# Performance work log

Measured on AMD Instinct MI355X. Metric: run time of the kernel, lower is better.

## Reference

```python
import jax, jax.numpy as jnp
import numpy as np

B, M, T = 4, 80, 65536
R, D, S, L = 64, 64, 64, 20  # residual, dilation, skip channels; num_layers


def setup_inputs() -> dict:
    key = jax.random.key(0)
    ks = jax.random.split(key, 14)

    def w(k, shape, fan_in):
        return jax.random.normal(k, shape, jnp.float32) * (1.0 / np.sqrt(fan_in))

    return {
        "x": jax.random.normal(ks[0], (B, M, T), jnp.float32),
        # causal 1x1 conv: Conv1d(M, R, 1) -> weight [R, M]
        "w_causal": w(ks[1], (R, M), M),
        "b_causal": jnp.zeros((R,), jnp.float32),
        # per-layer stacked weights (kernel_size=1 so all convs are channel matmuls)
        "w_dil": w(ks[2], (L, D, R), R),
        "b_dil": jnp.zeros((L, D), jnp.float32),
        "w_res": w(ks[3], (L, R, D), D),
        "b_res": jnp.zeros((L, R), jnp.float32),
        "w_skip": w(ks[4], (L, S, D), D),
        "b_skip": jnp.zeros((L, S), jnp.float32),
        "w_post1": w(ks[5], (S, S), S),
        "b_post1": jnp.zeros((S,), jnp.float32),
        "w_post2": w(ks[6], (1, S), S),
        "b_post2": jnp.zeros((1,), jnp.float32),
    }


def reference(x, w_causal, b_causal, w_dil, b_dil, w_res, b_res,
              w_skip, b_skip, w_post1, b_post1, w_post2, b_post2):
    # initial 1x1 conv: [B,M,T] -> [B,R,T]
    h = jnp.einsum('rm,bmt->brt', w_causal, x) + b_causal[None, :, None]

    skip0 = jnp.zeros((x.shape[0], w_skip.shape[1], x.shape[2]), x.dtype)

    def layer(carry, params):
        h, skip_sum = carry
        wd, bd, wr, br, ws, bs = params
        f = jnp.tanh(jnp.einsum('dr,brt->bdt', wd, h) + bd[None, :, None])
        skip_sum = skip_sum + jnp.einsum('sd,bdt->bst', ws, f) + bs[None, :, None]
        h = h + jnp.einsum('rd,bdt->brt', wr, f) + br[None, :, None]
        return (h, skip_sum), None

    (h, skip_sum), _ = jax.lax.scan(
        layer, (h, skip0), (w_dil, b_dil, w_res, b_res, w_skip, b_skip))

    s = jnp.tanh(skip_sum)
    s = jnp.tanh(jnp.einsum('os,bst->bot', w_post1, s) + b_post1[None, :, None])
    out = jnp.einsum('os,bst->bot', w_post2, s) + b_post2[None, :, None]
    return out[:, 0, :]  # squeeze channel dim -> [B, T]
```

## Files before the change

kernel.cpp:

```cpp
#include <hip/hip_runtime.h>

#define NB 4
#define NM 80
#define NT 65536
#define NL 20

typedef __bf16 bf16x8 __attribute__((ext_vector_type(8), may_alias));
typedef float f32x4 __attribute__((ext_vector_type(4), may_alias));
typedef unsigned int u32x2 __attribute__((ext_vector_type(2), may_alias));
typedef unsigned int u32x4 __attribute__((ext_vector_type(4), may_alias));

#define WCHI 491520
#define WCLO 497664
#define W1HI 503808
#define W1LO 507904

__device__ __forceinline__ unsigned f2u(float x) { return __float_as_uint(x); }
__device__ __forceinline__ float u2f(unsigned u) { return __uint_as_float(u); }
__device__ __forceinline__ unsigned pack2(float a, float b) {
    return (f2u(a) >> 16) | (f2u(b) & 0xffff0000u);
}
__device__ __forceinline__ unsigned rne_hi(float a) {
    unsigned u = f2u(a);
    return (u + 0x7fffu + ((u >> 16) & 1u)) & 0xffff0000u;
}
__device__ __forceinline__ unsigned pack2_rne(float a, float b) {
    return (rne_hi(a) >> 16) | rne_hi(b);
}
__device__ __forceinline__ float fast_tanh(float v) {
    float e = __expf(2.0f * v);
    return 1.0f - 2.0f / (e + 1.0f);
}
__device__ __forceinline__ f32x4 mm3(bf16x8 ah, bf16x8 al, bf16x8 bh, bf16x8 bl, f32x4 c) {
    c = __builtin_amdgcn_mfma_f32_16x16x32_bf16(ah, bh, c, 0, 0, 0);
    c = __builtin_amdgcn_mfma_f32_16x16x32_bf16(ah, bl, c, 0, 0, 0);
    c = __builtin_amdgcn_mfma_f32_16x16x32_bf16(al, bh, c, 0, 0, 0);
    return c;
}
__device__ __forceinline__ f32x4 mm2(bf16x8 ah, bf16x8 al, bf16x8 b, f32x4 c) {
    c = __builtin_amdgcn_mfma_f32_16x16x32_bf16(ah, b, c, 0, 0, 0);
    c = __builtin_amdgcn_mfma_f32_16x16x32_bf16(al, b, c, 0, 0, 0);
    return c;
}
__device__ __forceinline__ void split_pack(f32x4 v, u32x2& hi, u32x2& lo) {
    float l0 = v[0] - u2f(f2u(v[0]) & 0xffff0000u);
    float l1 = v[1] - u2f(f2u(v[1]) & 0xffff0000u);
    float l2 = v[2] - u2f(f2u(v[2]) & 0xffff0000u);
    float l3 = v[3] - u2f(f2u(v[3]) & 0xffff0000u);
    hi[0] = pack2(v[0], v[1]);
    hi[1] = pack2(v[2], v[3]);
    lo[0] = pack2(l0, l1);
    lo[1] = pack2(l2, l3);
}
__device__ __forceinline__ unsigned shf(unsigned v, int sl) {
    return (unsigned)__shfl((int)v, sl, 64);
}
__device__ __forceinline__ u32x4 gatherB(u32x2 p0, u32x2 p1, int slA, int slB, bool hiSel) {
    unsigned a0 = shf(p0[0], slA), b0 = shf(p1[0], slA);
    unsigned a1 = shf(p0[1], slA), b1 = shf(p1[1], slA);
    unsigned a2 = shf(p0[0], slB), b2 = shf(p1[0], slB);
    unsigned a3 = shf(p0[1], slB), b3 = shf(p1[1], slB);
    u32x4 r;
    r[0] = hiSel ? b0 : a0;
    r[1] = hiSel ? b1 : a1;
    r[2] = hiSel ? b2 : a2;
    r[3] = hiSel ? b3 : a3;
    return r;
}
__device__ __forceinline__ bf16x8 asbf(const u32x4& v) { return *(const bf16x8*)&v; }

__device__ __forceinline__ void stage_phase(const unsigned short* __restrict__ wsu,
                                            unsigned short* lbase, int pg, int wave, int lane) {
#pragma unroll
    for (int jj = 0; jj < 4; ++jj) {
        const unsigned short* g = wsu + (size_t)pg * 8192 + (wave * 4 + jj) * 512 + lane * 8;
        unsigned short* lp = lbase + (wave * 4 + jj) * 512;
        __builtin_amdgcn_global_load_lds(
            (const __attribute__((address_space(1))) unsigned int*)g,
            (__attribute__((address_space(3))) unsigned int*)lp, 16, 0, 0);
    }
}

#define PHASE_SYNC() do { \
    asm volatile("s_waitcnt vmcnt(0)" ::: "memory"); \
    __builtin_amdgcn_s_barrier(); \
} while (0)

extern "C" __global__ void __launch_bounds__(256)
wavenet_prep(const float* __restrict__ wc, const float* __restrict__ wd,
             const float* __restrict__ wsk, const float* __restrict__ wr,
             const float* __restrict__ w1, unsigned short* __restrict__ o)
{
    int i = blockIdx.x * 256 + threadIdx.x;
    if (i < 491520) {
        int pg = i >> 13;
        int within = i & 8191;
        int c = within >> 9;
        int lam = (within >> 3) & 63;
        int j = i & 7;
        int plane = c >> 3, m = (c >> 1) & 3, ks = c & 1;
        int row = m * 16 + (lam & 15);
        int k = ks * 32 + (lam >> 4) * 8 + j;
        int l = pg / 3, p = pg - 3 * l;
        const float* W = (p == 0) ? wd : (p == 1) ? wsk : wr;
        float v = W[(l * 64 + row) * 64 + k];
        unsigned uh = f2u(v) & 0xffff0000u;
        unsigned val = plane ? (f2u(v - u2f(uh)) >> 16) : (uh >> 16);
        o[i] = (unsigned short)val;
    } else if (i < 497664) {
        int idx = i - 491520;
        int r = idx / 96, mm = idx - r * 96;
        float v = (mm < NM) ? wc[r * NM + mm] : 0.0f;
        unsigned uh = f2u(v) & 0xffff0000u;
        o[WCHI + idx] = (unsigned short)(uh >> 16);
        o[WCLO + idx] = (unsigned short)(f2u(v - u2f(uh)) >> 16);
    } else if (i < 501760) {
        int idx = i - 497664;
        float v = w1[idx];
        unsigned uh = f2u(v) & 0xffff0000u;
        o[W1HI + idx] = (unsigned short)(uh >> 16);
        o[W1LO + idx] = (unsigned short)(f2u(v - u2f(uh)) >> 16);
    }
}

extern "C" __global__ void __launch_bounds__(256)
wavenet_mfma(const float* __restrict__ x, const float* __restrict__ bc,
             const float* __restrict__ bd, const float* __restrict__ br,
             const float* __restrict__ bs, const float* __restrict__ b1,
             const float* __restrict__ w2, const float* __restrict__ b2,
             const unsigned short* __restrict__ wsu, float* __restrict__ out)
{
    __shared__ __align__(16) unsigned short wbuf[2][8192];

    const int tid = threadIdx.x;
    const int wave = tid >> 6;
    const int lane = tid & 63;
    const int q = lane >> 4;
    const int c16 = lane & 15;
    const int wcol0 = wave * 32;

    const int slA = ((lane & 16) << 1) + c16;
    const int slB = slA + 16;
    const bool hiSel = lane >= 32;

    const int gcol0 = blockIdx.x * 128;
    const int bidx = gcol0 >> 16;
    const float* xbase = x + (size_t)bidx * NM * NT + (gcol0 & (NT - 1));

    stage_phase(wsu, &wbuf[0][0], 0, wave, lane);

    f32x4 h[4][2];
    f32x4 skipacc[4][2];
#pragma unroll
    for (int m = 0; m < 4; ++m)
#pragma unroll
        for (int nt = 0; nt < 2; ++nt)
            skipacc[m][nt] = (f32x4){0.f, 0.f, 0.f, 0.f};

#pragma unroll
    for (int nt = 0; nt < 2; ++nt) {
        const int colL = wcol0 + nt * 16 + c16;
        const float* xcp = xbase + colL;

        bf16x8 Bh[3], Bl[3];
#pragma unroll
        for (int ks = 0; ks < 3; ++ks) {
            u32x4 ph, pl;
#pragma unroll
            for (int w = 0; w < 4; ++w) {
                const int m0 = ks * 32 + q * 8 + 2 * w;
                float a, bv;
                if (ks < 2) {
                    a  = xcp[(size_t)m0 * NT];
                    bv = xcp[(size_t)(m0 + 1) * NT];
                } else {
                    const int ma = (m0 < NM) ? m0 : 0;
                    const int mb = (m0 + 1 < NM) ? (m0 + 1) : 0;
                    a  = (m0 < NM) ? xcp[(size_t)ma * NT] : 0.0f;
                    bv = (m0 + 1 < NM) ? xcp[(size_t)mb * NT] : 0.0f;
                }
                const float la = a - u2f(f2u(a) & 0xffff0000u);
                const float lb = bv - u2f(f2u(bv) & 0xffff0000u);
                ph[w] = pack2(a, bv);
                pl[w] = pack2(la, lb);
            }
            Bh[ks] = asbf(ph);
            Bl[ks] = asbf(pl);
        }

#pragma unroll
        for (int m = 0; m < 4; ++m) {
            f32x4 acc = *(const f32x4*)(bc + m * 16 + q * 4);
#pragma unroll
            for (int ks = 0; ks < 3; ++ks) {
                bf16x8 Ah = *(const bf16x8*)(wsu + WCHI + (m * 16 + c16) * 96 + ks * 32 + q * 8);
                bf16x8 Al = *(const bf16x8*)(wsu + WCLO + (m * 16 + c16) * 96 + ks * 32 + q * 8);
                acc = mm3(Ah, Al, Bh[ks], Bl[ks], acc);
            }
            h[m][nt] = acc;
        }
    }

    int buf = 0;
#pragma unroll 1
    for (int l = 0; l < NL; ++l) {
        const float* bdl = bd + l * 64;
        const float* brl = br + l * 64;

        PHASE_SYNC();
        stage_phase(wsu, &wbuf[buf ^ 1][0], 3 * l + 1, wave, lane);
        {
            const unsigned short* wb = &wbuf[buf][0];

            u32x4 BhH[2][2], BlH[2][2];
#pragma unroll
            for (int nt = 0; nt < 2; ++nt) {
                u32x2 Ph[4], Pl[4];
#pragma unroll
                for (int m = 0; m < 4; ++m) split_pack(h[m][nt], Ph[m], Pl[m]);
#pragma unroll
                for (int ks = 0; ks < 2; ++ks) {
                    BhH[nt][ks] = gatherB(Ph[ks * 2], Ph[ks * 2 + 1], slA, slB, hiSel);
                    BlH[nt][ks] = gatherB(Pl[ks * 2], Pl[ks * 2 + 1], slA, slB, hiSel);
                }
            }

            u32x2 Pf[2][4];
#pragma unroll
            for (int m = 0; m < 4; ++m) {
                bf16x8 Ah[2], Al[2];
#pragma unroll
                for (int ks = 0; ks < 2; ++ks) {
                    Ah[ks] = *(const bf16x8*)(wb + (m * 2 + ks) * 512 + lane * 8);
                    Al[ks] = *(const bf16x8*)(wb + (8 * 8 + (m * 2 + ks) * 8 - 8 * 8 + 8 * 512 / 512 * 0 + (8 + m * 2 + ks) * 512 - (m * 2 + ks) * 512 - 512 * 8) * 0 + (8 + m * 2 + ks) * 512 + lane * 8);
                }
                f32x4 bd4 = *(const f32x4*)(bdl + m * 16 + q * 4);
#pragma unroll
                for (int nt = 0; nt < 2; ++nt) {
                    f32x4 acc = bd4;
#pragma unroll
                    for (int ks = 0; ks < 2; ++ks)
                        acc = mm3(Ah[ks], Al[ks], asbf(BhH[nt][ks]), asbf(BlH[nt][ks]), acc);
                    Pf[nt][m][0] = pack2_rne(fast_tanh(acc[0]), fast_tanh(acc[1]));
                    Pf[nt][m][1] = pack2_rne(fast_tanh(acc[2]), fast_tanh(acc[3]));
                }
            }
            buf ^= 1;

            u32x4 BF[2][2];
#pragma unroll
            for (int nt = 0; nt < 2; ++nt)
#pragma unroll
                for (int ks = 0; ks < 2; ++ks)
                    BF[nt][ks] = gatherB(Pf[nt][ks * 2], Pf[nt][ks * 2 + 1], slA, slB, hiSel);

            PHASE_SYNC();
            stage_phase(wsu, &wbuf[buf ^ 1][0], 3 * l + 2, wave, lane);
            wb = &wbuf[buf][0];
#pragma unroll
            for (int m = 0; m < 4; ++m) {
                bf16x8 Ah[2], Al[2];
#pragma unroll
                for (int ks = 0; ks < 2; ++ks) {
                    Ah[ks] = *(const bf16x8*)(wb + (m * 2 + ks) * 512 + lane * 8);
                    Al[ks] = *(const bf16x8*)(wb + (8 + m * 2 + ks) * 512 + lane * 8);
                }
#pragma unroll
                for (int nt = 0; nt < 2; ++nt)
#pragma unroll
                    for (int ks = 0; ks < 2; ++ks)
                        skipacc[m][nt] = mm2(Ah[ks], Al[ks], asbf(BF[nt][ks]), skipacc[m][nt]);
            }
            buf ^= 1;

            PHASE_SYNC();
            if (l < NL - 1)
                stage_phase(wsu, &wbuf[buf ^ 1][0], 3 * l + 3, wave, lane);
            wb = &wbuf[buf][0];
#pragma unroll
            for (int m = 0; m < 4; ++m) {
                bf16x8 Ah[2], Al[2];
#pragma unroll
                for (int ks = 0; ks < 2; ++ks) {
                    Ah[ks] = *(const bf16x8*)(wb + (m * 2 + ks) * 512 + lane * 8);
                    Al[ks] = *(const bf16x8*)(wb + (8 + m * 2 + ks) * 512 + lane * 8);
                }
                f32x4 br4 = *(const f32x4*)(brl + m * 16 + q * 4);
#pragma unroll
                for (int nt = 0; nt < 2; ++nt) {
                    f32x4 c = h[m][nt];
#pragma unroll
                    for (int i = 0; i < 4; ++i) c[i] += br4[i];
#pragma unroll
                    for (int ks = 0; ks < 2; ++ks)
                        c = mm2(Ah[ks], Al[ks], asbf(BF[nt][ks]), c);
                    h[m][nt] = c;
                }
            }
            buf ^= 1;
        }
    }

    u32x2 Ps[2][4];
#pragma unroll
    for (int m = 0; m < 4; ++m) {
        f32x4 bsum = (f32x4){0.f, 0.f, 0.f, 0.f};
#pragma unroll
        for (int l = 0; l < NL; ++l) {
            f32x4 bv = *(const f32x4*)(bs + l * 64 + m * 16 + q * 4);
#pragma unroll
            for (int i = 0; i < 4; ++i) bsum[i] += bv[i];
        }
#pragma unroll
        for (int nt = 0; nt < 2; ++nt) {
            Ps[nt][m][0] = pack2_rne(fast_tanh(skipacc[m][nt][0] + bsum[0]),
                                     fast_tanh(skipacc[m][nt][1] + bsum[1]));
            Ps[nt][m][1] = pack2_rne(fast_tanh(skipacc[m][nt][2] + bsum[2]),
                                     fast_tanh(skipacc[m][nt][3] + bsum[3]));
        }
    }
    u32x4 BS[2][2];
#pragma unroll
    for (int nt = 0; nt < 2; ++nt)
#pragma unroll
        for (int ks = 0; ks < 2; ++ks)
            BS[nt][ks] = gatherB(Ps[nt][ks * 2], Ps[nt][ks * 2 + 1], slA, slB, hiSel);

    f32x4 s2a[4][2];
#pragma unroll
    for (int m = 0; m < 4; ++m) {
        bf16x8 Ah[2], Al[2];
#pragma unroll
        for (int ks = 0; ks < 2; ++ks) {
            Ah[ks] = *(const bf16x8*)(wsu + W1HI + (m * 16 + c16) * 64 + ks * 32 + q * 8);
            Al[ks] = *(const bf16x8*)(wsu + W1LO + (m * 16 + c16) * 64 + ks * 32 + q * 8);
        }
        f32x4 b14 = *(const f32x4*)(b1 + m * 16 + q * 4);
#pragma unroll
        for (int nt = 0; nt < 2; ++nt) {
            f32x4 acc = b14;
#pragma unroll
            for (int ks = 0; ks < 2; ++ks)
                acc = mm2(Ah[ks], Al[ks], asbf(BS[nt][ks]), acc);
#pragma unroll
            for (int i = 0; i < 4; ++i) s2a[m][nt][i] = fast_tanh(acc[i]);
        }
    }

    f32x4 w24[4];
#pragma unroll
    for (int m = 0; m < 4; ++m) w24[m] = *(const f32x4*)(w2 + m * 16 + q * 4);
    const float b2v = b2[0];
#pragma unroll
    for (int nt = 0; nt < 2; ++nt) {
        float p = 0.0f;
#pragma unroll
        for (int m = 0; m < 4; ++m)
#pragma unroll
            for (int i = 0; i < 4; ++i)
                p = fmaf(w24[m][i], s2a[m][nt][i], p);
        p += __shfl_xor(p, 16);
        p += __shfl_xor(p, 32);
        if (q == 0)
            out[gcol0 + wcol0 + nt * 16 + c16] = b2v + p;
    }
}

extern "C" void kernel_launch(void* const* d_in, const int* in_sizes, int n_in,
                              void* d_out, int out_size, void* d_ws, size_t ws_size,
                              hipStream_t stream) {
    const float* x  = (const float*)d_in[0];
    const float* wc = (const float*)d_in[1];
    const float* bc = (const float*)d_in[2];
    const float* wd = (const float*)d_in[3];
    const float* bd = (const float*)d_in[4];
    const float* wr = (const float*)d_in[5];
    const float* br = (const float*)d_in[6];
    const float* ws = (const float*)d_in[7];
    const float* bs = (const float*)d_in[8];
    const float* w1 = (const float*)d_in[9];
    const float* b1 = (const float*)d_in[10];
    const float* w2 = (const float*)d_in[11];
    const float* b2 = (const float*)d_in[12];
    float* out = (float*)d_out;
    unsigned short* wsu = (unsigned short*)d_ws;

    hipLaunchKernelGGL(wavenet_prep, dim3(1960), dim3(256), 0, stream,
                       wc, wd, ws, wr, w1, wsu);
    hipLaunchKernelGGL(wavenet_mfma, dim3((NB * NT) / 128), dim3(256), 0, stream,
                       x, bc, bd, br, bs, b1, w2, b2, wsu, out);
}
```

Measured before the change: 645.0 us.

## Halve per-wave column tile, use hardware bf16 pack, raise waves per EU

Each wave now handles 16 time columns instead of 32, so the block covers 64 columns and the grid doubles. This cuts register-resident h/skip accumulators in half so more waves can be resident (with an amdgpu_waves_per_eu hint), trading away reuse of the weight fragments loaded from shared memory across two column tiles. The hi/lo split now uses v_cvt_pk_bf16_f32 (round-to-nearest hi) instead of truncation masks. Weight staging into LDS per block is now amortized over half as many columns, increasing LDS traffic and barrier count per output.

```diff
diff --git a/kernel.cpp b/kernel.cpp
--- a/kernel.cpp
+++ b/kernel.cpp
@@ -26,6 +26,11 @@
 }
 __device__ __forceinline__ unsigned pack2_rne(float a, float b) {
     return (rne_hi(a) >> 16) | rne_hi(b);
+}
+__device__ __forceinline__ unsigned cvtpk(float a, float b) {
+    unsigned r;
+    asm("v_cvt_pk_bf16_f32 %0, %1, %2" : "=v"(r) : "v"(a), "v"(b));
+    return r;
 }
 __device__ __forceinline__ float fast_tanh(float v) {
     float e = __expf(2.0f * v);
@@ -43,14 +48,14 @@
     return c;
 }
 __device__ __forceinline__ void split_pack(f32x4 v, u32x2& hi, u32x2& lo) {
-    float l0 = v[0] - u2f(f2u(v[0]) & 0xffff0000u);
-    float l1 = v[1] - u2f(f2u(v[1]) & 0xffff0000u);
-    float l2 = v[2] - u2f(f2u(v[2]) & 0xffff0000u);
-    float l3 = v[3] - u2f(f2u(v[3]) & 0xffff0000u);
-    hi[0] = pack2(v[0], v[1]);
-    hi[1] = pack2(v[2], v[3]);
-    lo[0] = pack2(l0, l1);
-    lo[1] = pack2(l2, l3);
+    hi[0] = cvtpk(v[0], v[1]);
+    hi[1] = cvtpk(v[2], v[3]);
+    float r0 = v[0] - u2f(hi[0] << 16);
+    float r1 = v[1] - u2f(hi[0] & 0xffff0000u);
+    float r2 = v[2] - u2f(hi[1] << 16);
+    float r3 = v[3] - u2f(hi[1] & 0xffff0000u);
+    lo[0] = cvtpk(r0, r1);
+    lo[1] = cvtpk(r2, r3);
 }
 __device__ __forceinline__ unsigned shf(unsigned v, int sl) {
     return (unsigned)__shfl((int)v, sl, 64);
@@ -124,6 +129,7 @@
 }
 
 extern "C" __global__ void __launch_bounds__(256)
+__attribute__((amdgpu_waves_per_eu(3, 4)))
 wavenet_mfma(const float* __restrict__ x, const float* __restrict__ bc,
              const float* __restrict__ bd, const float* __restrict__ br,
              const float* __restrict__ bs, const float* __restrict__ b1,
@@ -137,29 +143,25 @@
     const int lane = tid & 63;
     const int q = lane >> 4;
     const int c16 = lane & 15;
-    const int wcol0 = wave * 32;
+    const int wcol0 = wave * 16;
 
     const int slA = ((lane & 16) << 1) + c16;
     const int slB = slA + 16;
     const bool hiSel = lane >= 32;
 
-    const int gcol0 = blockIdx.x * 128;
+    const int gcol0 = blockIdx.x * 64;
     const int bidx = gcol0 >> 16;
     const float* xbase = x + (size_t)bidx * NM * NT + (gcol0 & (NT - 1));
 
     stage_phase(wsu, &wbuf[0][0], 0, wave, lane);
 
-    f32x4 h[4][2];
-    f32x4 skipacc[4][2];
-#pragma unroll
-    for (int m = 0; m < 4; ++m)
-#pragma unroll
-        for (int nt = 0; nt < 2; ++nt)
-            skipacc[m][nt] = (f32x4){0.f, 0.f, 0.f, 0.f};
-
-#pragma unroll
-    for (int nt = 0; nt < 2; ++nt) {
-        const int colL = wcol0 + nt * 16 + c16;
+    f32x4 h[4];
+    f32x4 skipacc[4];
+#pragma unroll
+    for (int m = 0; m < 4; ++m) skipacc[m] = (f32x4){0.f, 0.f, 0.f, 0.f};
+
+    {
+        const int colL = wcol0 + c16;
         const float* xcp = xbase + colL;
 
         bf16x8 Bh[3], Bl[3];
@@ -197,7 +199,7 @@
                 bf16x8 Al = *(const bf16x8*)(wsu + WCLO + (m * 16 + c16) * 96 + ks * 32 + q * 8);
                 acc = mm3(Ah, Al, Bh[ks], Bl[ks], acc);
             }
-            h[m][nt] = acc;
+            h[m] = acc;
         }
     }
 
@@ -212,47 +214,40 @@
         {
             const unsigned short* wb = &wbuf[buf][0];
 
-            u32x4 BhH[2][2], BlH[2][2];
-#pragma unroll
-            for (int nt = 0; nt < 2; ++nt) {
+            u32x4 BhH[2], BlH[2];
+            {
                 u32x2 Ph[4], Pl[4];
 #pragma unroll
-                for (int m = 0; m < 4; ++m) split_pack(h[m][nt], Ph[m], Pl[m]);
+                for (int m = 0; m < 4; ++m) split_pack(h[m], Ph[m], Pl[m]);
 #pragma unroll
                 for (int ks = 0; ks < 2; ++ks) {
-                    BhH[nt][ks] = gatherB(Ph[ks * 2], Ph[ks * 2 + 1], slA, slB, hiSel);
-                    BlH[nt][ks] = gatherB(Pl[ks * 2], Pl[ks * 2 + 1], slA, slB, hiSel);
-                }
-            }
-
-            u32x2 Pf[2][4];
+                    BhH[ks] = gatherB(Ph[ks * 2], Ph[ks * 2 + 1], slA, slB, hiSel);
+                    BlH[ks] = gatherB(Pl[ks * 2], Pl[ks * 2 + 1], slA, slB, hiSel);
+                }
+            }
+
+            u32x2 Pf[4];
 #pragma unroll
             for (int m = 0; m < 4; ++m) {
                 bf16x8 Ah[2], Al[2];
 #pragma unroll
                 for (int ks = 0; ks < 2; ++ks) {
                     Ah[ks] = *(const bf16x8*)(wb + (m * 2 + ks) * 512 + lane * 8);
-                    Al[ks] = *(const bf16x8*)(wb + (8 * 8 + (m * 2 + ks) * 8 - 8 * 8 + 8 * 512 / 512 * 0 + (8 + m * 2 + ks) * 512 - (m * 2 + ks) * 512 - 512 * 8) * 0 + (8 + m * 2 + ks) * 512 + lane * 8);
-                }
-                f32x4 bd4 = *(const f32x4*)(bdl + m * 16 + q * 4);
-#pragma unroll
-                for (int nt = 0; nt < 2; ++nt) {
-                    f32x4 acc = bd4;
-#pragma unroll
-                    for (int ks = 0; ks < 2; ++ks)
-                        acc = mm3(Ah[ks], Al[ks], asbf(BhH[nt][ks]), asbf(BlH[nt][ks]), acc);
-                    Pf[nt][m][0] = pack2_rne(fast_tanh(acc[0]), fast_tanh(acc[1]));
-                    Pf[nt][m][1] = pack2_rne(fast_tanh(acc[2]), fast_tanh(acc[3]));
-                }
+                    Al[ks] = *(const bf16x8*)(wb + (8 + m * 2 + ks) * 512 + lane * 8);
+                }
+                f32x4 acc = *(const f32x4*)(bdl + m * 16 + q * 4);
+#pragma unroll
+                for (int ks = 0; ks < 2; ++ks)
+                    acc = mm3(Ah[ks], Al[ks], asbf(BhH[ks]), asbf(BlH[ks]), acc);
+                Pf[m][0] = pack2_rne(fast_tanh(acc[0]), fast_tanh(acc[1]));
+                Pf[m][1] = pack2_rne(fast_tanh(acc[2]), fast_tanh(acc[3]));
             }
             buf ^= 1;
 
-            u32x4 BF[2][2];
-#pragma unroll
-            for (int nt = 0; nt < 2; ++nt)
-#pragma unroll
-                for (int ks = 0; ks < 2; ++ks)
-                    BF[nt][ks] = gatherB(Pf[nt][ks * 2], Pf[nt][ks * 2 + 1], slA, slB, hiSel);
+            u32x4 BF[2];
+#pragma unroll
+            for (int ks = 0; ks < 2; ++ks)
+                BF[ks] = gatherB(Pf[ks * 2], Pf[ks * 2 + 1], slA, slB, hiSel);
 
             PHASE_SYNC();
             stage_phase(wsu, &wbuf[buf ^ 1][0], 3 * l + 2, wave, lane);
@@ -266,10 +261,8 @@
                     Al[ks] = *(const bf16x8*)(wb + (8 + m * 2 + ks) * 512 + lane * 8);
                 }
 #pragma unroll
-                for (int nt = 0; nt < 2; ++nt)
-#pragma unroll
-                    for (int ks = 0; ks < 2; ++ks)
-                        skipacc[m][nt] = mm2(Ah[ks], Al[ks], asbf(BF[nt][ks]), skipacc[m][nt]);
+                for (int ks = 0; ks < 2; ++ks)
+                    skipacc[m] = mm2(Ah[ks], Al[ks], asbf(BF[ks]), skipacc[m]);
             }
             buf ^= 1;
 
@@ -286,22 +279,19 @@
                     Al[ks] = *(const bf16x8*)(wb + (8 + m * 2 + ks) * 512 + lane * 8);
                 }
                 f32x4 br4 = *(const f32x4*)(brl + m * 16 + q * 4);
-#pragma unroll
-                for (int nt = 0; nt < 2; ++nt) {
-                    f32x4 c = h[m][nt];
-#pragma unroll
-                    for (int i = 0; i < 4; ++i) c[i] += br4[i];
-#pragma unroll
-                    for (int ks = 0; ks < 2; ++ks)
-                        c = mm2(Ah[ks], Al[ks], asbf(BF[nt][ks]), c);
-                    h[m][nt] = c;
-                }
+                f32x4 c = h[m];
+#pragma unroll
+                for (int i = 0; i < 4; ++i) c[i] += br4[i];
+#pragma unroll
+                for (int ks = 0; ks < 2; ++ks)
+                    c = mm2(Ah[ks], Al[ks], asbf(BF[ks]), c);
+                h[m] = c;
             }
             buf ^= 1;
         }
     }
 
-    u32x2 Ps[2][4];
+    u32x2 Ps[4];
 #pragma unroll
     for (int m = 0; m < 4; ++m) {
         f32x4 bsum = (f32x4){0.f, 0.f, 0.f, 0.f};
@@ -311,22 +301,17 @@
 #pragma unroll
             for (int i = 0; i < 4; ++i) bsum[i] += bv[i];
         }
-#pragma unroll
-        for (int nt = 0; nt < 2; ++nt) {
-            Ps[nt][m][0] = pack2_rne(fast_tanh(skipacc[m][nt][0] + bsum[0]),
-                                     fast_tanh(skipacc[m][nt][1] + bsum[1]));
-            Ps[nt][m][1] = pack2_rne(fast_tanh(skipacc[m][nt][2] + bsum[2]),
-                                     fast_tanh(skipacc[m][nt][3] + bsum[3]));
-        }
-    }
-    u32x4 BS[2][2];
-#pragma unroll
-    for (int nt = 0; nt < 2; ++nt)
-#pragma unroll
-        for (int ks = 0; ks < 2; ++ks)
-            BS[nt][ks] = gatherB(Ps[nt][ks * 2], Ps[nt][ks * 2 + 1], slA, slB, hiSel);
-
-    f32x4 s2a[4][2];
+        Ps[m][0] = pack2_rne(fast_tanh(skipacc[m][0] + bsum[0]),
+                             fast_tanh(skipacc[m][1] + bsum[1]));
+        Ps[m][1] = pack2_rne(fast_tanh(skipacc[m][2] + bsum[2]),
+                             fast_tanh(skipacc[m][3] + bsum[3]));
+    }
+    u32x4 BS[2];
+#pragma unroll
+    for (int ks = 0; ks < 2; ++ks)
+        BS[ks] = gatherB(Ps[ks * 2], Ps[ks * 2 + 1], slA, slB, hiSel);
+
+    f32x4 s2a[4];
 #pragma unroll
     for (int m = 0; m < 4; ++m) {
         bf16x8 Ah[2], Al[2];
@@ -335,35 +320,28 @@
             Ah[ks] = *(const bf16x8*)(wsu + W1HI + (m * 16 + c16) * 64 + ks * 32 + q * 8);
             Al[ks] = *(const bf16x8*)(wsu + W1LO + (m * 16 + c16) * 64 + ks * 32 + q * 8);
         }
-        f32x4 b14 = *(const f32x4*)(b1 + m * 16 + q * 4);
-#pragma unroll
-        for (int nt = 0; nt < 2; ++nt) {
-            f32x4 acc = b14;
-#pragma unroll
-            for (int ks = 0; ks < 2; ++ks)
-                acc = mm2(Ah[ks], Al[ks], asbf(BS[nt][ks]), acc);
-#pragma unroll
-            for (int i = 0; i < 4; ++i) s2a[m][nt][i] = fast_tanh(acc[i]);
-        }
+        f32x4 acc = *(const f32x4*)(b1 + m * 16 + q * 4);
+#pragma unroll
+        for (int ks = 0; ks < 2; ++ks)
+            acc = mm2(Ah[ks], Al[ks], asbf(BS[ks]), acc);
+#pragma unroll
+        for (int i = 0; i < 4; ++i) s2a[m][i] = fast_tanh(acc[i]);
     }
 
     f32x4 w24[4];
 #pragma unroll
     for (int m = 0; m < 4; ++m) w24[m] = *(const f32x4*)(w2 + m * 16 + q * 4);
     const float b2v = b2[0];
-#pragma unroll
-    for (int nt = 0; nt < 2; ++nt) {
-        float p = 0.0f;
-#pragma unroll
-        for (int m = 0; m < 4; ++m)
-#pragma unroll
-            for (int i = 0; i < 4; ++i)
-                p = fmaf(w24[m][i], s2a[m][nt][i], p);
-        p += __shfl_xor(p, 16);
-        p += __shfl_xor(p, 32);
-        if (q == 0)
-            out[gcol0 + wcol0 + nt * 16 + c16] = b2v + p;
-    }
+    float p = 0.0f;
+#pragma unroll
+    for (int m = 0; m < 4; ++m)
+#pragma unroll
+        for (int i = 0; i < 4; ++i)
+            p = fmaf(w24[m][i], s2a[m][i], p);
+    p += __shfl_xor(p, 16);
+    p += __shfl_xor(p, 32);
+    if (q == 0)
+        out[gcol0 + wcol0 + c16] = b2v + p;
 }
 
 extern "C" void kernel_launch(void* const* d_in, const int* in_sizes, int n_in,
@@ -387,6 +365,6 @@
 
     hipLaunchKernelGGL(wavenet_prep, dim3(1960), dim3(256), 0, stream,
                        wc, wd, ws, wr, w1, wsu);
-    hipLaunchKernelGGL(wavenet_mfma, dim3((NB * NT) / 128), dim3(256), 0, stream,
+    hipLaunchKernelGGL(wavenet_mfma, dim3((NB * NT) / 64), dim3(256), 0, stream,
                        x, bc, bd, br, bs, b1, w2, b2, wsu, out);
 }
```

After: 677.1 us. 1.05x slower.

## Use hardware bf16 packing, drop skip low-plane MFMAs, raise occupancy bound

Applied to the files above, without the earlier changes.

The hi/lo split now uses the hardware v_cvt_pk_bf16_f32 conversion, and the weight prep rounds to nearest even instead of truncating. With the high part rounded, dropping the low plane of the skip weights costs less accuracy. The skip-projection phase therefore stages only the high plane and does one MFMA per tile instead of two. Launch bounds now request 4 blocks per CU. This cuts MFMA count, LDS traffic and ALU work for splitting, at the cost of lower precision in the skip path and more register pressure from the occupancy hint.

```diff
diff --git a/kernel.cpp b/kernel.cpp
--- a/kernel.cpp
+++ b/kernel.cpp
@@ -26,6 +26,11 @@
 }
 __device__ __forceinline__ unsigned pack2_rne(float a, float b) {
     return (rne_hi(a) >> 16) | rne_hi(b);
+}
+__device__ __forceinline__ unsigned cvtpk(float a, float b) {
+    unsigned r;
+    asm("v_cvt_pk_bf16_f32 %0, %1, %2" : "=v"(r) : "v"(a), "v"(b));
+    return r;
 }
 __device__ __forceinline__ float fast_tanh(float v) {
     float e = __expf(2.0f * v);
@@ -43,14 +48,14 @@
     return c;
 }
 __device__ __forceinline__ void split_pack(f32x4 v, u32x2& hi, u32x2& lo) {
-    float l0 = v[0] - u2f(f2u(v[0]) & 0xffff0000u);
-    float l1 = v[1] - u2f(f2u(v[1]) & 0xffff0000u);
-    float l2 = v[2] - u2f(f2u(v[2]) & 0xffff0000u);
-    float l3 = v[3] - u2f(f2u(v[3]) & 0xffff0000u);
-    hi[0] = pack2(v[0], v[1]);
-    hi[1] = pack2(v[2], v[3]);
-    lo[0] = pack2(l0, l1);
-    lo[1] = pack2(l2, l3);
+    hi[0] = cvtpk(v[0], v[1]);
+    hi[1] = cvtpk(v[2], v[3]);
+    float r0 = v[0] - u2f(hi[0] << 16);
+    float r1 = v[1] - u2f(hi[0] & 0xffff0000u);
+    float r2 = v[2] - u2f(hi[1] << 16);
+    float r3 = v[3] - u2f(hi[1] & 0xffff0000u);
+    lo[0] = cvtpk(r0, r1);
+    lo[1] = cvtpk(r2, r3);
 }
 __device__ __forceinline__ unsigned shf(unsigned v, int sl) {
     return (unsigned)__shfl((int)v, sl, 64);
@@ -69,12 +74,13 @@
 }
 __device__ __forceinline__ bf16x8 asbf(const u32x4& v) { return *(const bf16x8*)&v; }
 
+template <int NCH>
 __device__ __forceinline__ void stage_phase(const unsigned short* __restrict__ wsu,
                                             unsigned short* lbase, int pg, int wave, int lane) {
 #pragma unroll
-    for (int jj = 0; jj < 4; ++jj) {
-        const unsigned short* g = wsu + (size_t)pg * 8192 + (wave * 4 + jj) * 512 + lane * 8;
-        unsigned short* lp = lbase + (wave * 4 + jj) * 512;
+    for (int jj = 0; jj < NCH; ++jj) {
+        const unsigned short* g = wsu + (size_t)pg * 8192 + (wave * NCH + jj) * 512 + lane * 8;
+        unsigned short* lp = lbase + (wave * NCH + jj) * 512;
         __builtin_amdgcn_global_load_lds(
             (const __attribute__((address_space(1))) unsigned int*)g,
             (__attribute__((address_space(3))) unsigned int*)lp, 16, 0, 0);
@@ -104,26 +110,26 @@
         int l = pg / 3, p = pg - 3 * l;
         const float* W = (p == 0) ? wd : (p == 1) ? wsk : wr;
         float v = W[(l * 64 + row) * 64 + k];
-        unsigned uh = f2u(v) & 0xffff0000u;
+        unsigned uh = rne_hi(v);
         unsigned val = plane ? (f2u(v - u2f(uh)) >> 16) : (uh >> 16);
         o[i] = (unsigned short)val;
     } else if (i < 497664) {
         int idx = i - 491520;
         int r = idx / 96, mm = idx - r * 96;
         float v = (mm < NM) ? wc[r * NM + mm] : 0.0f;
-        unsigned uh = f2u(v) & 0xffff0000u;
+        unsigned uh = rne_hi(v);
         o[WCHI + idx] = (unsigned short)(uh >> 16);
         o[WCLO + idx] = (unsigned short)(f2u(v - u2f(uh)) >> 16);
     } else if (i < 501760) {
         int idx = i - 497664;
         float v = w1[idx];
-        unsigned uh = f2u(v) & 0xffff0000u;
+        unsigned uh = rne_hi(v);
         o[W1HI + idx] = (unsigned short)(uh >> 16);
         o[W1LO + idx] = (unsigned short)(f2u(v - u2f(uh)) >> 16);
     }
 }
 
-extern "C" __global__ void __launch_bounds__(256)
+extern "C" __global__ void __launch_bounds__(256, 4)
 wavenet_mfma(const float* __restrict__ x, const float* __restrict__ bc,
              const float* __restrict__ bd, const float* __restrict__ br,
              const float* __restrict__ bs, const float* __restrict__ b1,
@@ -147,7 +153,7 @@
     const int bidx = gcol0 >> 16;
     const float* xbase = x + (size_t)bidx * NM * NT + (gcol0 & (NT - 1));
 
-    stage_phase(wsu, &wbuf[0][0], 0, wave, lane);
+    stage_phase<4>(wsu, &wbuf[0][0], 0, wave, lane);
 
     f32x4 h[4][2];
     f32x4 skipacc[4][2];
@@ -208,7 +214,7 @@
         const float* brl = br + l * 64;
 
         PHASE_SYNC();
-        stage_phase(wsu, &wbuf[buf ^ 1][0], 3 * l + 1, wave, lane);
+        stage_phase<2>(wsu, &wbuf[buf ^ 1][0], 3 * l + 1, wave, lane);
         {
             const unsigned short* wb = &wbuf[buf][0];
 
@@ -232,7 +238,7 @@
 #pragma unroll
                 for (int ks = 0; ks < 2; ++ks) {
                     Ah[ks] = *(const bf16x8*)(wb + (m * 2 + ks) * 512 + lane * 8);
-                    Al[ks] = *(const bf16x8*)(wb + (8 * 8 + (m * 2 + ks) * 8 - 8 * 8 + 8 * 512 / 512 * 0 + (8 + m * 2 + ks) * 512 - (m * 2 + ks) * 512 - 512 * 8) * 0 + (8 + m * 2 + ks) * 512 + lane * 8);
+                    Al[ks] = *(const bf16x8*)(wb + (8 + m * 2 + ks) * 512 + lane * 8);
                 }
                 f32x4 bd4 = *(const f32x4*)(bdl + m * 16 + q * 4);
 #pragma unroll
@@ -255,27 +261,26 @@
                     BF[nt][ks] = gatherB(Pf[nt][ks * 2], Pf[nt][ks * 2 + 1], slA, slB, hiSel);
 
             PHASE_SYNC();
-            stage_phase(wsu, &wbuf[buf ^ 1][0], 3 * l + 2, wave, lane);
+            stage_phase<4>(wsu, &wbuf[buf ^ 1][0], 3 * l + 2, wave, lane);
             wb = &wbuf[buf][0];
 #pragma unroll
             for (int m = 0; m < 4; ++m) {
-                bf16x8 Ah[2], Al[2];
-#pragma unroll
-                for (int ks = 0; ks < 2; ++ks) {
+                bf16x8 Ah[2];
+#pragma unroll
+                for (int ks = 0; ks < 2; ++ks)
                     Ah[ks] = *(const bf16x8*)(wb + (m * 2 + ks) * 512 + lane * 8);
-                    Al[ks] = *(const bf16x8*)(wb + (8 + m * 2 + ks) * 512 + lane * 8);
-                }
 #pragma unroll
                 for (int nt = 0; nt < 2; ++nt)
 #pragma unroll
                     for (int ks = 0; ks < 2; ++ks)
-                        skipacc[m][nt] = mm2(Ah[ks], Al[ks], asbf(BF[nt][ks]), skipacc[m][nt]);
+                        skipacc[m][nt] = __builtin_amdgcn_mfma_f32_16x16x32_bf16(
+                            Ah[ks], asbf(BF[nt][ks]), skipacc[m][nt], 0, 0, 0);
             }
             buf ^= 1;
 
             PHASE_SYNC();
             if (l < NL - 1)
-                stage_phase(wsu, &wbuf[buf ^ 1][0], 3 * l + 3, wave, lane);
+                stage_phase<4>(wsu, &wbuf[buf ^ 1][0], 3 * l + 3, wave, lane);
             wb = &wbuf[buf][0];
 #pragma unroll
             for (int m = 0; m < 4; ++m) {
```

Measured after the change: 593.9 us. -7.9%, faster.
